# Kernel tuning notes

Hardware: AMD Instinct MI355X
Metric: run time of the kernel (lower is better)

## Reference

```python
import jax, jax.numpy as jnp
import numpy as np

B, S = 128, 32
C = [4, 8, 16, 32]
DN = ('NDHWC', 'DHWIO', 'NDHWC')


def _conv(x, w, stride=1, pad=None):
    k = w.shape[0]
    if pad is None:
        pad = [((k - 1) // 2, k // 2)] * 3  # k=3 -> (1,1); k=4 -> (1,2) as in scn even-kernel convention
    return jax.lax.conv_general_dilated(x, w, (stride,) * 3, pad, dimension_numbers=DN)


def _bn_relu(x, g, b, mask, eps=1e-4):
    # BatchNormLeakyReLU with leakiness=0 (ReLU); stats over ACTIVE voxels only, per channel
    cnt = jnp.maximum(mask.sum(), 1.0)
    mean = (x * mask).sum(axis=(0, 1, 2, 3)) / cnt
    var = (((x - mean) ** 2) * mask).sum(axis=(0, 1, 2, 3)) / cnt
    y = (x - mean) * jax.lax.rsqrt(var + eps) * g + b
    return jnp.maximum(y, 0.0) * mask


def _pool_mask(m):
    # scn.Convolution k=2 s=2: output site active iff any input in its 2^3 receptive field is active
    return jax.lax.reduce_window(m, 0.0, jax.lax.max, (1, 2, 2, 2, 1), (1, 2, 2, 2, 1), 'VALID')


def _up_mask(m):
    # scn.FullConvolution k=2 s=2: each active input activates its full 2^3 output block
    return jnp.repeat(jnp.repeat(jnp.repeat(m, 2, 1), 2, 2), 2, 3)


def _encoder(vox, maskraw, wp, enc, dec, wo):
    mask = (maskraw == 0).astype(vox.dtype)
    x = vox * mask
    x = _conv(x, wp) * mask  # prepare: submanifold conv 1 -> m=4
    for (g, b, ws, wd) in enc:  # 3 non-empty encoding stages (i < num_strides-1)
        x = _bn_relu(x, g, b, mask)
        x = _conv(x, ws) * mask               # submanifold conv k=3
        x = _conv(x, wd, stride=2, pad=[(0, 0)] * 3)  # strided Convolution k=2 s=2
        mask = _pool_mask(mask)
        x = x * mask
    # SparseToDense + view(-1, C*s^3) in NCDHW layout
    hidden = jnp.transpose(x, (0, 4, 1, 2, 3)).reshape(x.shape[0], -1)
    for (g, b, wu, ws3, ws4) in dec:  # i = 2, 1, 0
        x = _bn_relu(x, g, b, mask)
        x = jax.lax.conv_transpose(x, wu, (2, 2, 2), 'VALID', dimension_numbers=DN)  # FullConvolution
        mask = _up_mask(mask)
        x = x * mask
        x = _conv(x, ws3) * mask              # submanifold conv k=3 (end of decoding_conv1)
        mask = mask * (x[..., :1] > 0).astype(x.dtype)  # SparsifyFCS (applied twice; idempotent)
        x = x * mask
        x = _conv(x, ws4) * mask              # submanifold conv k=4 (decoding_conv2)
    out = _conv(x, wo) * mask                 # output: submanifold conv m -> 1
    return hidden, out


def setup_inputs():
    key = jax.random.key(0)
    ks = iter(jax.random.split(key, 64))

    def rnd(shape, s=0.1):
        return jax.random.normal(next(ks), shape, jnp.float32) * s

    inp = {}
    inp['vox'] = jax.random.normal(next(ks), (B, S, S, S, 1), jnp.float32)
    inp['maskraw'] = jax.random.randint(next(ks), (B, S, S, S, 1), 0, 10, jnp.int32)
    inp['wp'] = rnd((3, 3, 3, 1, C[0]))
    for i in range(3):
        ci, co = C[i], C[i + 1]
        inp[f'g_e{i}'] = 1.0 + rnd((ci,))
        inp[f'b_e{i}'] = rnd((ci,))
        inp[f'ws_e{i}'] = rnd((3, 3, 3, ci, ci))
        inp[f'wd_e{i}'] = rnd((2, 2, 2, ci, co))
    for j, i in enumerate([2, 1, 0]):
        ci, co = C[i + 1], C[i]
        inp[f'g_d{j}'] = 1.0 + rnd((ci,))
        inp[f'b_d{j}'] = rnd((ci,))
        inp[f'wu_d{j}'] = rnd((2, 2, 2, ci, co))
        inp[f'ws3_d{j}'] = rnd((3, 3, 3, co, co))
        inp[f'ws4_d{j}'] = rnd((4, 4, 4, co, co))
    inp['wo'] = rnd((3, 3, 3, C[0], 1))
    return inp


def reference(vox, maskraw, wp, g_e0, b_e0, ws_e0, wd_e0, g_e1, b_e1, ws_e1, wd_e1, g_e2, b_e2, ws_e2, wd_e2, g_d0, b_d0, wu_d0, ws3_d0, ws4_d0, g_d1, b_d1, wu_d1, ws3_d1, ws4_d1, g_d2, b_d2, wu_d2, ws3_d2, ws4_d2, wo):
    enc = [(g_e0, b_e0, ws_e0, wd_e0), (g_e1, b_e1, ws_e1, wd_e1), (g_e2, b_e2, ws_e2, wd_e2)]
    dec = [(g_d0, b_d0, wu_d0, ws3_d0, ws4_d0), (g_d1, b_d1, wu_d1, ws3_d1, ws4_d1), (g_d2, b_d2, wu_d2, ws3_d2, ws4_d2)]
    return _encoder(vox, maskraw, wp, enc, dec, wo)
```

## Files before the change

kernel.cpp:

```cpp
#include <hip/hip_runtime.h>

using u8 = unsigned char;

__global__ void mask_init_k(const int* __restrict__ mr, u8* __restrict__ m, int N) {
    int i = blockIdx.x * blockDim.x + threadIdx.x;
    if (i < N) m[i] = (mr[i] == 0) ? 1 : 0;
}

template <int SO>
__global__ void pool_k(const u8* __restrict__ mi, u8* __restrict__ mo) {
    const int N = 128 * SO * SO * SO;
    constexpr int SI = 2 * SO;
    int v = blockIdx.x * blockDim.x + threadIdx.x;
    if (v >= N) return;
    int t = v;
    int x = t % SO; t /= SO;
    int y = t % SO; t /= SO;
    int z = t % SO;
    int n = t / SO;
    u8 m = 0;
    for (int kd = 0; kd < 2; kd++)
        for (int kh = 0; kh < 2; kh++)
            for (int kw = 0; kw < 2; kw++)
                m |= mi[((n * SI + 2 * z + kd) * SI + 2 * y + kh) * SI + 2 * x + kw];
    mo[v] = m;
}


__global__ void prep4t_k(const float* __restrict__ vox, const u8* __restrict__ m,
                         const float* __restrict__ wp, float* __restrict__ out) {
    __shared__ float til[6 * 10 * 35];
    int bid = blockIdx.x;
    int y0 = (bid & 3) << 3, z0 = ((bid >> 2) & 7) << 2, n = bid >> 5;
    for (int t = threadIdx.x; t < 6 * 10 * 35; t += 256) {
        int x_ = t % 35;
        int rr = t / 35;
        int yy = rr % 10, zz = rr / 10;
        int gx = x_ - 1, gy = y0 + yy - 1, gz = z0 + zz - 1;
        float v = 0.f;
        if ((unsigned)gx < 32u && (unsigned)gy < 32u && (unsigned)gz < 32u) {
            int gi = ((n * 32 + gz) * 32 + gy) * 32 + gx;
            if (m[gi]) v = vox[gi];
        }
        til[t] = v;
    }
    __syncthreads();
    int tx = threadIdx.x;
    int xg = tx & 7, ly = (tx >> 3) & 7, lz = tx >> 6;
    int xb = xg << 2;
    int vbase = ((n * 32 + z0 + lz) * 32 + y0 + ly) * 32 + xb;
    u8 om[4];
#pragma unroll
    for (int j = 0; j < 4; j++) om[j] = m[vbase + j];
    float acc[4][4];
#pragma unroll
    for (int j = 0; j < 4; j++)
#pragma unroll
        for (int co = 0; co < 4; co++) acc[j][co] = 0.f;
    for (int kd = 0; kd < 3; kd++) {
        for (int kh = 0; kh < 3; kh++) {
            const float* rowp = &til[((lz + kd) * 10 + ly + kh) * 35 + xb];
            float col[6];
#pragma unroll
            for (int c = 0; c < 6; c++) col[c] = rowp[c];
            const float* wrow = wp + ((kd * 3 + kh) * 3) * 4;
#pragma unroll
            for (int kw = 0; kw < 3; kw++) {
                const float* wt = wrow + kw * 4;
#pragma unroll
                for (int j = 0; j < 4; j++) {
                    float xv = col[j + kw];
#pragma unroll
                    for (int co = 0; co < 4; co++) acc[j][co] += xv * wt[co];
                }
            }
        }
    }
#pragma unroll
    for (int j = 0; j < 4; j++)
#pragma unroll
        for (int co = 0; co < 4; co++)
            out[(size_t)(vbase + j) * 4 + co] = om[j] ? acc[j][co] : 0.f;
}

__global__ void convbn4t_k(const float* __restrict__ in, const float* __restrict__ w,
                           const u8* __restrict__ mask, const double* __restrict__ params,
                           float* __restrict__ out) {
    __shared__ float4 til[6 * 10 * 35];
    float sc[4], sh[4];
#pragma unroll
    for (int c = 0; c < 4; c++) { sc[c] = (float)params[c]; sh[c] = (float)params[4 + c]; }
    int bid = blockIdx.x;
    int y0 = (bid & 3) << 3, z0 = ((bid >> 2) & 7) << 2, n = bid >> 5;
    for (int t = threadIdx.x; t < 6 * 10 * 35; t += 256) {
        int x_ = t % 35;
        int rr = t / 35;
        int yy = rr % 10, zz = rr / 10;
        int gx = x_ - 1, gy = y0 + yy - 1, gz = z0 + zz - 1;
        float4 v = make_float4(0.f, 0.f, 0.f, 0.f);
        if ((unsigned)gx < 32u && (unsigned)gy < 32u && (unsigned)gz < 32u) {
            int gi = ((n * 32 + gz) * 32 + gy) * 32 + gx;
            if (mask[gi]) {
                float4 r = *(const float4*)(in + (size_t)gi * 4);
                v.x = fmaxf(r.x * sc[0] + sh[0], 0.f);
                v.y = fmaxf(r.y * sc[1] + sh[1], 0.f);
                v.z = fmaxf(r.z * sc[2] + sh[2], 0.f);
                v.w = fmaxf(r.w * sc[3] + sh[3], 0.f);
            }
        }
        til[t] = v;
    }
    __syncthreads();
    int tx = threadIdx.x;
    int xg = tx & 7, ly = (tx >> 3) & 7, lz = tx >> 6;
    int xb = xg << 2;
    int vbase = ((n * 32 + z0 + lz) * 32 + y0 + ly) * 32 + xb;
    u8 om[4];
#pragma unroll
    for (int j = 0; j < 4; j++) om[j] = mask[vbase + j];
    float acc[4][4];
#pragma unroll
    for (int j = 0; j < 4; j++)
#pragma unroll
        for (int co = 0; co < 4; co++) acc[j][co] = 0.f;
    for (int kd = 0; kd < 3; kd++) {
        for (int kh = 0; kh < 3; kh++) {
            const float4* rowp = &til[((lz + kd) * 10 + ly + kh) * 35 + xb];
            float col[6][4];
#pragma unroll
            for (int c = 0; c < 6; c++) {
                float4 t4 = rowp[c];
                col[c][0] = t4.x; col[c][1] = t4.y; col[c][2] = t4.z; col[c][3] = t4.w;
            }
            const float* wrow = w + ((kd * 3 + kh) * 3) * 16;
#pragma unroll
            for (int kw = 0; kw < 3; kw++) {
                const float* wt = wrow + kw * 16;
#pragma unroll
                for (int j = 0; j < 4; j++) {
#pragma unroll
                    for (int ci = 0; ci < 4; ci++) {
                        float xv = col[j + kw][ci];
#pragma unroll
                        for (int co = 0; co < 4; co++) acc[j][co] += xv * wt[ci * 4 + co];
                    }
                }
            }
        }
    }
#pragma unroll
    for (int j = 0; j < 4; j++)
#pragma unroll
        for (int co = 0; co < 4; co++)
            out[(size_t)(vbase + j) * 4 + co] = om[j] ? acc[j][co] : 0.f;
}

__global__ void conv3s4t_k(const float* __restrict__ in, const float* __restrict__ w,
                           const u8* __restrict__ pmask, u8* __restrict__ nmask,
                           float* __restrict__ out, double delta) {
    __shared__ float4 til[6 * 10 * 35];
    int bid = blockIdx.x;
    int y0 = (bid & 3) << 3, z0 = ((bid >> 2) & 7) << 2, n = bid >> 5;
    for (int t = threadIdx.x; t < 6 * 10 * 35; t += 256) {
        int x_ = t % 35;
        int rr = t / 35;
        int yy = rr % 10, zz = rr / 10;
        int gx = x_ - 1, gy = y0 + yy - 1, gz = z0 + zz - 1;
        float4 v = make_float4(0.f, 0.f, 0.f, 0.f);
        if ((unsigned)gx < 32u && (unsigned)gy < 32u && (unsigned)gz < 32u)
            v = *(const float4*)(in + (size_t)(((n * 32 + gz) * 32 + gy) * 32 + gx) * 4);
        til[t] = v;
    }
    __syncthreads();
    int tx = threadIdx.x;
    int xg = tx & 7, ly = (tx >> 3) & 7, lz = tx >> 6;
    int xb = xg << 2;
    int gy = y0 + ly, gz = z0 + lz;
    int vbase = ((n * 32 + gz) * 32 + gy) * 32 + xb;
    int pbase = ((n * 16 + (gz >> 1)) * 16 + (gy >> 1)) * 16 + (xb >> 1);
    u8 pm[4];
    pm[0] = pm[1] = pmask[pbase];
    pm[2] = pm[3] = pmask[pbase + 1];
    double acc0[4], asum[4];
    float accf[4][4];
#pragma unroll
    for (int j = 0; j < 4; j++) {
        acc0[j] = 0.0; asum[j] = 0.0;
#pragma unroll
        for (int co = 0; co < 4; co++) accf[j][co] = 0.f;
    }
    for (int kd = 0; kd < 3; kd++) {
        for (int kh = 0; kh < 3; kh++) {
            const float4* rowp = &til[((lz + kd) * 10 + ly + kh) * 35 + xb];
            float col[6][4];
#pragma unroll
            for (int c = 0; c < 6; c++) {
                float4 t4 = rowp[c];
                col[c][0] = t4.x; col[c][1] = t4.y; col[c][2] = t4.z; col[c][3] = t4.w;
            }
            const float* wrow = w + ((kd * 3 + kh) * 3) * 16;
#pragma unroll
            for (int kw = 0; kw < 3; kw++) {
                const float* wt = wrow + kw * 16;
#pragma unroll
                for (int j = 0; j < 4; j++) {
#pragma unroll
                    for (int ci = 0; ci < 4; ci++) {
                        float xv = col[j + kw][ci];
                        double term = (double)xv * (double)wt[ci * 4 + 0];
                        acc0[j] += term;
                        asum[j] += fabs(term);
#pragma unroll
                        for (int co = 1; co < 4; co++) accf[j][co] += xv * wt[ci * 4 + co];
                    }
                }
            }
        }
    }
#pragma unroll
    for (int j = 0; j < 4; j++) {
        u8 nm = (pm[j] && (acc0[j] > -delta * asum[j])) ? 1 : 0;
        nmask[vbase + j] = nm;
        out[(size_t)(vbase + j) * 4 + 0] = nm ? (float)acc0[j] : 0.f;
#pragma unroll
        for (int co = 1; co < 4; co++) out[(size_t)(vbase + j) * 4 + co] = nm ? accf[j][co] : 0.f;
    }
}

__global__ void conv4x4t_k(const float* __restrict__ in, const float* __restrict__ w,
                           const u8* __restrict__ outmask, float* __restrict__ out) {
    __shared__ float4 til[7 * 11 * 35];
    int bid = blockIdx.x;
    int y0 = (bid & 3) << 3, z0 = ((bid >> 2) & 7) << 2, n = bid >> 5;
    for (int t = threadIdx.x; t < 7 * 11 * 35; t += 256) {
        int x_ = t % 35;
        int rr = t / 35;
        int yy = rr % 11, zz = rr / 11;
        int gx = x_ - 1, gy = y0 + yy - 1, gz = z0 + zz - 1;
        float4 v = make_float4(0.f, 0.f, 0.f, 0.f);
        if ((unsigned)gx < 32u && (unsigned)gy < 32u && (unsigned)gz < 32u)
            v = *(const float4*)(in + (size_t)(((n * 32 + gz) * 32 + gy) * 32 + gx) * 4);
        til[t] = v;
    }
    __syncthreads();
    int tx = threadIdx.x;
    int xg = tx & 7, ly = (tx >> 3) & 7, lz = tx >> 6;
    int xb = xg << 2;
    int vbase = ((n * 32 + z0 + lz) * 32 + y0 + ly) * 32 + xb;
    u8 om[4];
#pragma unroll
    for (int j = 0; j < 4; j++) om[j] = outmask[vbase + j];
    float acc[4][4];
#pragma unroll
    for (int j = 0; j < 4; j++)
#pragma unroll
        for (int co = 0; co < 4; co++) acc[j][co] = 0.f;
    for (int kd = 0; kd < 4; kd++) {
        for (int kh = 0; kh < 4; kh++) {
            const float4* rowp = &til[((lz + kd) * 11 + ly + kh) * 35 + xb];
            float col[7][4];
#pragma unroll
            for (int c = 0; c < 7; c++) {
                float4 t4 = rowp[c];
                col[c][0] = t4.x; col[c][1] = t4.y; col[c][2] = t4.z; col[c][3] = t4.w;
            }
            const float* wrow = w + ((kd * 4 + kh) * 4) * 16;
#pragma unroll
            for (int kw = 0; kw < 4; kw++) {
                const float* wt = wrow + kw * 16;
#pragma unroll
                for (int j = 0; j < 4; j++) {
#pragma unroll
                    for (int ci = 0; ci < 4; ci++) {
                        float xv = col[j + kw][ci];
#pragma unroll
                        for (int co = 0; co < 4; co++) acc[j][co] += xv * wt[ci * 4 + co];
                    }
                }
            }
        }
    }
#pragma unroll
    for (int j = 0; j < 4; j++)
#pragma unroll
        for (int co = 0; co < 4; co++)
            out[(size_t)(vbase + j) * 4 + co] = om[j] ? acc[j][co] : 0.f;
}

__global__ void outconv4t_k(const float* __restrict__ in, const float* __restrict__ w,
                            const u8* __restrict__ mask, float* __restrict__ out) {
    __shared__ float4 til[6 * 10 * 35];
    int bid = blockIdx.x;
    int y0 = (bid & 3) << 3, z0 = ((bid >> 2) & 7) << 2, n = bid >> 5;
    for (int t = threadIdx.x; t < 6 * 10 * 35; t += 256) {
        int x_ = t % 35;
        int rr = t / 35;
        int yy = rr % 10, zz = rr / 10;
        int gx = x_ - 1, gy = y0 + yy - 1, gz = z0 + zz - 1;
        float4 v = make_float4(0.f, 0.f, 0.f, 0.f);
        if ((unsigned)gx < 32u && (unsigned)gy < 32u && (unsigned)gz < 32u)
            v = *(const float4*)(in + (size_t)(((n * 32 + gz) * 32 + gy) * 32 + gx) * 4);
        til[t] = v;
    }
    __syncthreads();
    int tx = threadIdx.x;
    int xg = tx & 7, ly = (tx >> 3) & 7, lz = tx >> 6;
    int xb = xg << 2;
    int vbase = ((n * 32 + z0 + lz) * 32 + y0 + ly) * 32 + xb;
    u8 om[4];
#pragma unroll
    for (int j = 0; j < 4; j++) om[j] = mask[vbase + j];
    float acc[4] = {0.f, 0.f, 0.f, 0.f};
    for (int kd = 0; kd < 3; kd++) {
        for (int kh = 0; kh < 3; kh++) {
            const float4* rowp = &til[((lz + kd) * 10 + ly + kh) * 35 + xb];
            float col[6][4];
#pragma unroll
            for (int c = 0; c < 6; c++) {
                float4 t4 = rowp[c];
                col[c][0] = t4.x; col[c][1] = t4.y; col[c][2] = t4.z; col[c][3] = t4.w;
            }
            const float* wrow = w + ((kd * 3 + kh) * 3) * 4;
#pragma unroll
            for (int kw = 0; kw < 3; kw++) {
                const float* wt = wrow + kw * 4;
#pragma unroll
                for (int j = 0; j < 4; j++) {
#pragma unroll
                    for (int ci = 0; ci < 4; ci++) acc[j] += col[j + kw][ci] * wt[ci];
                }
            }
        }
    }
#pragma unroll
    for (int j = 0; j < 4; j++) out[vbase + j] = om[j] ? acc[j] : 0.f;
}


__global__ void convbn8_k(const float* __restrict__ in, const float* __restrict__ w,
                          const u8* __restrict__ mask, const double* __restrict__ params,
                          float* __restrict__ out) {
    __shared__ float til[3 * 10 * 11 * 16];
    float sc[16], sh[16];
#pragma unroll
    for (int c = 0; c < 16; c++) { sc[c] = (float)params[c]; sh[c] = (float)params[16 + c]; }
    int z = blockIdx.x & 7, n = blockIdx.x >> 3;
    for (int t = threadIdx.x; t < 300; t += 64) {
        int xx = t % 10;
        int rr = t / 10;
        int yy = rr % 10, zz = rr / 10;
        int gx = xx - 1, gy = yy - 1, gz = z + zz - 1;
        float v[16];
#pragma unroll
        for (int c = 0; c < 16; c++) v[c] = 0.f;
        if ((unsigned)gx < 8u && (unsigned)gy < 8u && (unsigned)gz < 8u) {
            int gi = ((n * 8 + gz) * 8 + gy) * 8 + gx;
            if (mask[gi]) {
                const float* ip = in + (size_t)gi * 16;
#pragma unroll
                for (int c = 0; c < 16; c++) v[c] = fmaxf(ip[c] * sc[c] + sh[c], 0.f);
            }
        }
        float* dst = &til[((zz * 10 + yy) * 11 + xx) * 16];
#pragma unroll
        for (int k = 0; k < 4; k++)
            ((float4*)dst)[k] = make_float4(v[4 * k], v[4 * k + 1], v[4 * k + 2], v[4 * k + 3]);
    }
    __syncthreads();
    int x = threadIdx.x & 7, y = threadIdx.x >> 3;
    int v = ((n * 8 + z) * 8 + y) * 8 + x;
    u8 om = mask[v];
    float acc[16];
#pragma unroll
    for (int co = 0; co < 16; co++) acc[co] = 0.f;
    for (int kd = 0; kd < 3; kd++) {
        for (int kh = 0; kh < 3; kh++) {
            const float* rp = &til[((kd * 10 + (y + kh)) * 11 + x) * 16];
#pragma unroll
            for (int kw = 0; kw < 3; kw++) {
                const float* xp = rp + kw * 16;
                const float* wt = w + ((kd * 3 + kh) * 3 + kw) * 256;
#pragma unroll
                for (int ci = 0; ci < 16; ci++) {
                    float xv = xp[ci];
#pragma unroll
                    for (int co = 0; co < 16; co++) acc[co] += xv * wt[ci * 16 + co];
                }
            }
        }
    }
#pragma unroll
    for (int co = 0; co < 16; co++) out[(size_t)v * 16 + co] = om ? acc[co] : 0.f;
}

__global__ void conv3s8_k(const float* __restrict__ in, const float* __restrict__ w,
                          const u8* __restrict__ pmask, u8* __restrict__ nmask,
                          float* __restrict__ out, double delta) {
    __shared__ float til[3 * 10 * 11 * 16];
    int z = blockIdx.x & 7, n = blockIdx.x >> 3;
    for (int t = threadIdx.x; t < 300; t += 64) {
        int xx = t % 10;
        int rr = t / 10;
        int yy = rr % 10, zz = rr / 10;
        int gx = xx - 1, gy = yy - 1, gz = z + zz - 1;
        float4 v0 = make_float4(0.f, 0.f, 0.f, 0.f), v1 = v0, v2 = v0, v3 = v0;
        if ((unsigned)gx < 8u && (unsigned)gy < 8u && (unsigned)gz < 8u) {
            const float4* ip = (const float4*)(in + (size_t)(((n * 8 + gz) * 8 + gy) * 8 + gx) * 16);
            v0 = ip[0]; v1 = ip[1]; v2 = ip[2]; v3 = ip[3];
        }
        float4* dst = (float4*)&til[((zz * 10 + yy) * 11 + xx) * 16];
        dst[0] = v0; dst[1] = v1; dst[2] = v2; dst[3] = v3;
    }
    __syncthreads();
    int x = threadIdx.x & 7, y = threadIdx.x >> 3;
    int v = ((n * 8 + z) * 8 + y) * 8 + x;
    int pidx = ((n * 4 + (z >> 1)) * 4 + (y >> 1)) * 4 + (x >> 1);
    u8 pm = pmask[pidx];
    double acc0 = 0.0, asum = 0.0;
    float accf[16];
#pragma unroll
    for (int co = 0; co < 16; co++) accf[co] = 0.f;
    for (int kd = 0; kd < 3; kd++) {
        for (int kh = 0; kh < 3; kh++) {
            const float* rp = &til[((kd * 10 + (y + kh)) * 11 + x) * 16];
#pragma unroll
            for (int kw = 0; kw < 3; kw++) {
                const float* xp = rp + kw * 16;
                const float* wt = w + ((kd * 3 + kh) * 3 + kw) * 256;
#pragma unroll
                for (int ci = 0; ci < 16; ci++) {
                    float xv = xp[ci];
                    double term = (double)xv * (double)wt[ci * 16 + 0];
                    acc0 += term;
                    asum += fabs(term);
#pragma unroll
                    for (int co = 1; co < 16; co++) accf[co] += xv * wt[ci * 16 + co];
                }
            }
        }
    }
    u8 nm = (pm && (acc0 > -delta * asum)) ? 1 : 0;
    nmask[v] = nm;
    out[(size_t)v * 16 + 0] = nm ? (float)acc0 : 0.f;
#pragma unroll
    for (int co = 1; co < 16; co++) out[(size_t)v * 16 + co] = nm ? accf[co] : 0.f;
}

__global__ void conv48_k(const float* __restrict__ in, const float* __restrict__ w,
                         const u8* __restrict__ outmask, float* __restrict__ out) {
    __shared__ float til[4 * 11 * 13 * 16];
    int z = blockIdx.x & 7, n = blockIdx.x >> 3;
    for (int t = threadIdx.x; t < 484; t += 64) {
        int xx = t % 11;
        int rr = t / 11;
        int yy = rr % 11, zz = rr / 11;
        int gx = xx - 1, gy = yy - 1, gz = z + zz - 1;
        float4 v0 = make_float4(0.f, 0.f, 0.f, 0.f), v1 = v0, v2 = v0, v3 = v0;
        if ((unsigned)gx < 8u && (unsigned)gy < 8u && (unsigned)gz < 8u) {
            const float4* ip = (const float4*)(in + (size_t)(((n * 8 + gz) * 8 + gy) * 8 + gx) * 16);
            v0 = ip[0]; v1 = ip[1]; v2 = ip[2]; v3 = ip[3];
        }
        float4* dst = (float4*)&til[((zz * 11 + yy) * 13 + xx) * 16];
        dst[0] = v0; dst[1] = v1; dst[2] = v2; dst[3] = v3;
    }
    __syncthreads();
    int x = threadIdx.x & 7, y = threadIdx.x >> 3;
    int v = ((n * 8 + z) * 8 + y) * 8 + x;
    u8 om = outmask[v];
    float acc[16];
#pragma unroll
    for (int co = 0; co < 16; co++) acc[co] = 0.f;
    for (int kd = 0; kd < 4; kd++) {
        for (int kh = 0; kh < 4; kh++) {
            const float* rp = &til[((kd * 11 + (y + kh)) * 13 + x) * 16];
#pragma unroll
            for (int kw = 0; kw < 4; kw++) {
                const float* xp = rp + kw * 16;
                const float* wt = w + ((kd * 4 + kh) * 4 + kw) * 256;
#pragma unroll
                for (int ci = 0; ci < 16; ci++) {
                    float xv = xp[ci];
#pragma unroll
                    for (int co = 0; co < 16; co++) acc[co] += xv * wt[ci * 16 + co];
                }
            }
        }
    }
#pragma unroll
    for (int co = 0; co < 16; co++) out[(size_t)v * 16 + co] = om ? acc[co] : 0.f;
}


template <int K, int CIN, int COUT, int S>
__global__ void conv_k(const float* __restrict__ in, const float* __restrict__ w,
                       const u8* __restrict__ outmask, float* __restrict__ out) {
    const int N = 128 * S * S * S;
    int v = blockIdx.x * blockDim.x + threadIdx.x;
    if (v >= N) return;
    if (!outmask[v]) {
#pragma unroll
        for (int co = 0; co < COUT; co++) out[(size_t)v * COUT + co] = 0.f;
        return;
    }
    int t = v;
    int x = t % S; t /= S;
    int y = t % S; t /= S;
    int z = t % S;
    int n = t / S;
    float acc[COUT];
#pragma unroll
    for (int co = 0; co < COUT; co++) acc[co] = 0.f;
    constexpr int PLO = (K - 1) / 2;
    for (int kd = 0; kd < K; kd++) {
        int zz = z + kd - PLO; if ((unsigned)zz >= (unsigned)S) continue;
        for (int kh = 0; kh < K; kh++) {
            int yy = y + kh - PLO; if ((unsigned)yy >= (unsigned)S) continue;
            for (int kw = 0; kw < K; kw++) {
                int xx = x + kw - PLO; if ((unsigned)xx >= (unsigned)S) continue;
                int sv = ((n * S + zz) * S + yy) * S + xx;
                const float* ip = in + (size_t)sv * CIN;
                const float* wpk = w + ((kd * K + kh) * K + kw) * CIN * COUT;
#pragma unroll
                for (int ci = 0; ci < CIN; ci++) {
                    float xv = ip[ci];
#pragma unroll
                    for (int co = 0; co < COUT; co++) acc[co] += xv * wpk[ci * COUT + co];
                }
            }
        }
    }
#pragma unroll
    for (int co = 0; co < COUT; co++) out[(size_t)v * COUT + co] = acc[co];
}

template <int CIN, int COUT, int S>
__global__ void convbn_k(const float* __restrict__ in, const float* __restrict__ w,
                         const u8* __restrict__ mask, const double* __restrict__ params,
                         float* __restrict__ out) {
    const int N = 128 * S * S * S;
    int v = blockIdx.x * blockDim.x + threadIdx.x;
    if (v >= N) return;
    if (!mask[v]) {
#pragma unroll
        for (int co = 0; co < COUT; co++) out[(size_t)v * COUT + co] = 0.f;
        return;
    }
    int t = v;
    int x = t % S; t /= S;
    int y = t % S; t /= S;
    int z = t % S;
    int n = t / S;
    float sc[CIN], sh[CIN];
#pragma unroll
    for (int c = 0; c < CIN; c++) { sc[c] = (float)params[c]; sh[c] = (float)params[CIN + c]; }
    float acc[COUT];
#pragma unroll
    for (int co = 0; co < COUT; co++) acc[co] = 0.f;
    for (int kd = 0; kd < 3; kd++) {
        int zz = z + kd - 1; if ((unsigned)zz >= (unsigned)S) continue;
        for (int kh = 0; kh < 3; kh++) {
            int yy = y + kh - 1; if ((unsigned)yy >= (unsigned)S) continue;
            for (int kw = 0; kw < 3; kw++) {
                int xx = x + kw - 1; if ((unsigned)xx >= (unsigned)S) continue;
                int sv = ((n * S + zz) * S + yy) * S + xx;
                if (!mask[sv]) continue;
                const float* ip = in + (size_t)sv * CIN;
                const float* wpk = w + ((kd * 3 + kh) * 3 + kw) * CIN * COUT;
#pragma unroll
                for (int ci = 0; ci < CIN; ci++) {
                    float yv = fmaxf(ip[ci] * sc[ci] + sh[ci], 0.f);
#pragma unroll
                    for (int co = 0; co < COUT; co++) acc[co] += yv * wpk[ci * COUT + co];
                }
            }
        }
    }
#pragma unroll
    for (int co = 0; co < COUT; co++) out[(size_t)v * COUT + co] = acc[co];
}

template <int CIN, int COUT, int S>
__global__ void conv3s_k(const float* __restrict__ in, const float* __restrict__ w,
                         const u8* __restrict__ pmask, u8* __restrict__ nmask,
                         float* __restrict__ out, double delta) {
    const int N = 128 * S * S * S;
    constexpr int SP = S / 2;
    int v = blockIdx.x * blockDim.x + threadIdx.x;
    if (v >= N) return;
    int t = v;
    int x = t % S; t /= S;
    int y = t % S; t /= S;
    int z = t % S;
    int n = t / S;
    int pidx = ((n * SP + (z >> 1)) * SP + (y >> 1)) * SP + (x >> 1);
    if (!pmask[pidx]) {
        nmask[v] = 0;
#pragma unroll
        for (int co = 0; co < COUT; co++) out[(size_t)v * COUT + co] = 0.f;
        return;
    }
    double acc0 = 0.0, asum = 0.0;
    float acc[COUT];
#pragma unroll
    for (int co = 0; co < COUT; co++) acc[co] = 0.f;
    for (int kd = 0; kd < 3; kd++) {
        int zz = z + kd - 1; if ((unsigned)zz >= (unsigned)S) continue;
        for (int kh = 0; kh < 3; kh++) {
            int yy = y + kh - 1; if ((unsigned)yy >= (unsigned)S) continue;
            for (int kw = 0; kw < 3; kw++) {
                int xx = x + kw - 1; if ((unsigned)xx >= (unsigned)S) continue;
                int sv = ((n * S + zz) * S + yy) * S + xx;
                const float* ip = in + (size_t)sv * CIN;
                const float* wpk = w + ((kd * 3 + kh) * 3 + kw) * CIN * COUT;
#pragma unroll
                for (int ci = 0; ci < CIN; ci++) {
                    float xv = ip[ci];
                    double term = (double)xv * (double)wpk[ci * COUT + 0];
                    acc0 += term;
                    asum += fabs(term);
#pragma unroll
                    for (int co = 1; co < COUT; co++) acc[co] += xv * wpk[ci * COUT + co];
                }
            }
        }
    }
    u8 nm = (acc0 > -delta * asum) ? 1 : 0;
    nmask[v] = nm;
    out[(size_t)v * COUT + 0] = nm ? (float)acc0 : 0.f;
#pragma unroll
    for (int co = 1; co < COUT; co++) out[(size_t)v * COUT + co] = nm ? acc[co] : 0.f;
}

template <int CIN, int COUT, int SO>
__global__ void down_k(const float* __restrict__ in, const float* __restrict__ w,
                       const u8* __restrict__ outmask, float* __restrict__ out) {
    const int N = 128 * SO * SO * SO;
    constexpr int SI = 2 * SO;
    int v = blockIdx.x * blockDim.x + threadIdx.x;
    if (v >= N) return;
    if (!outmask[v]) {
#pragma unroll
        for (int co = 0; co < COUT; co++) out[(size_t)v * COUT + co] = 0.f;
        return;
    }
    int t = v;
    int x = t % SO; t /= SO;
    int y = t % SO; t /= SO;
    int z = t % SO;
    int n = t / SO;
    float acc[COUT];
#pragma unroll
    for (int co = 0; co < COUT; co++) acc[co] = 0.f;
    for (int kd = 0; kd < 2; kd++)
        for (int kh = 0; kh < 2; kh++)
            for (int kw = 0; kw < 2; kw++) {
                int sv = ((n * SI + 2 * z + kd) * SI + 2 * y + kh) * SI + 2 * x + kw;
                const float* ip = in + (size_t)sv * CIN;
                const float* wpk = w + ((kd * 2 + kh) * 2 + kw) * CIN * COUT;
#pragma unroll
                for (int ci = 0; ci < CIN; ci++) {
                    float xv = ip[ci];
#pragma unroll
                    for (int co = 0; co < COUT; co++) acc[co] += xv * wpk[ci * COUT + co];
                }
            }
#pragma unroll
    for (int co = 0; co < COUT; co++) out[(size_t)v * COUT + co] = acc[co];
}

template <int CIN, int COUT, int SI>
__global__ void upbn_k(const float* __restrict__ in, const float* __restrict__ w,
                       const u8* __restrict__ inmask, const double* __restrict__ params,
                       float* __restrict__ out) {
    constexpr int SO = 2 * SI;
    const int N = 128 * SO * SO * SO;
    int v = blockIdx.x * blockDim.x + threadIdx.x;
    if (v >= N) return;
    int t = v;
    int x = t % SO; t /= SO;
    int y = t % SO; t /= SO;
    int z = t % SO;
    int n = t / SO;
    int sv = ((n * SI + (z >> 1)) * SI + (y >> 1)) * SI + (x >> 1);
    if (!inmask[sv]) {
#pragma unroll
        for (int co = 0; co < COUT; co++) out[(size_t)v * COUT + co] = 0.f;
        return;
    }
    int tap = ((1 - (z & 1)) * 2 + (1 - (y & 1))) * 2 + (1 - (x & 1));
    const float* wpk = w + tap * CIN * COUT;
    const float* ip = in + (size_t)sv * CIN;
    float acc[COUT];
#pragma unroll
    for (int co = 0; co < COUT; co++) acc[co] = 0.f;
#pragma unroll
    for (int ci = 0; ci < CIN; ci++) {
        float yv = fmaxf(ip[ci] * (float)params[ci] + (float)params[CIN + ci], 0.f);
#pragma unroll
        for (int co = 0; co < COUT; co++) acc[co] += yv * wpk[ci * COUT + co];
    }
#pragma unroll
    for (int co = 0; co < COUT; co++) out[(size_t)v * COUT + co] = acc[co];
}

template <int C>
__global__ void bn_reduce_k(const float* __restrict__ x, const u8* __restrict__ m, int N,
                            double* __restrict__ partial) {
    double cnt = 0.0, sx[C], s2[C];
#pragma unroll
    for (int c = 0; c < C; c++) { sx[c] = 0.0; s2[c] = 0.0; }
    int stride = gridDim.x * blockDim.x;
    for (int v = blockIdx.x * blockDim.x + threadIdx.x; v < N; v += stride) {
        if (!m[v]) continue;
        cnt += 1.0;
#pragma unroll
        for (int c = 0; c < C; c++) {
            double xv = (double)x[(size_t)v * C + c];
            sx[c] += xv;
            s2[c] += xv * xv;
        }
    }
#pragma unroll
    for (int off = 32; off > 0; off >>= 1) {
        cnt += __shfl_down(cnt, off, 64);
#pragma unroll
        for (int c = 0; c < C; c++) {
            sx[c] += __shfl_down(sx[c], off, 64);
            s2[c] += __shfl_down(s2[c], off, 64);
        }
    }
    __shared__ double sbuf[4][2 * C + 1];
    int wave = threadIdx.x >> 6;
    if ((threadIdx.x & 63) == 0) {
        sbuf[wave][0] = cnt;
#pragma unroll
        for (int c = 0; c < C; c++) {
            sbuf[wave][1 + c] = sx[c];
            sbuf[wave][1 + C + c] = s2[c];
        }
    }
    __syncthreads();
    if (threadIdx.x == 0) {
        double* p = partial + (size_t)blockIdx.x * (2 * C + 1);
        double tcnt = 0.0;
        for (int wv = 0; wv < 4; wv++) tcnt += sbuf[wv][0];
        p[0] = tcnt;
#pragma unroll
        for (int c = 0; c < C; c++) {
            double a = 0.0, b = 0.0;
            for (int wv = 0; wv < 4; wv++) { a += sbuf[wv][1 + c]; b += sbuf[wv][1 + C + c]; }
            p[1 + c] = a;
            p[1 + C + c] = b;
        }
    }
}

template <int C>
__global__ void bn_final_k(const double* __restrict__ partial, int nblocks,
                           const float* __restrict__ g, const float* __restrict__ b,
                           double* __restrict__ params) {
    int c = threadIdx.x;
    if (c >= C) return;
    double cnt = 0.0, sx = 0.0, s2 = 0.0;
    for (int bk = 0; bk < nblocks; bk++) {
        const double* p = partial + (size_t)bk * (2 * C + 1);
        cnt += p[0];
        sx += p[1 + c];
        s2 += p[1 + C + c];
    }
    if (cnt < 1.0) cnt = 1.0;
    double mean = sx / cnt;
    double var = s2 / cnt - mean * mean;
    double sc = (double)g[c] / sqrt(var + 1e-4);
    params[c] = sc;
    params[C + c] = (double)b[c] - mean * sc;
}

__global__ void hidden_k(const float* __restrict__ x, float* __restrict__ out) {
    int i = blockIdx.x * blockDim.x + threadIdx.x;
    if (i >= 128 * 2048) return;
    int b = i >> 11;
    int r = i & 2047;
    int c = r >> 6;
    int s = r & 63;
    int d = s >> 4;
    int h = (s >> 2) & 3;
    int w = s & 3;
    out[i] = x[((((b * 4 + d) * 4 + h) * 4 + w) << 5) + c];
}

extern "C" void kernel_launch(void* const* d_in, const int* in_sizes, int n_in,
                              void* d_out, int out_size, void* d_ws, size_t ws_size,
                              hipStream_t stream) {
    const float* vox = (const float*)d_in[0];
    const int* mraw = (const int*)d_in[1];
    const float* wp = (const float*)d_in[2];
    const float* g_e0 = (const float*)d_in[3];
    const float* b_e0 = (const float*)d_in[4];
    const float* ws_e0 = (const float*)d_in[5];
    const float* wd_e0 = (const float*)d_in[6];
    const float* g_e1 = (const float*)d_in[7];
    const float* b_e1 = (const float*)d_in[8];
    const float* ws_e1 = (const float*)d_in[9];
    const float* wd_e1 = (const float*)d_in[10];
    const float* g_e2 = (const float*)d_in[11];
    const float* b_e2 = (const float*)d_in[12];
    const float* ws_e2 = (const float*)d_in[13];
    const float* wd_e2 = (const float*)d_in[14];
    const float* g_d0 = (const float*)d_in[15];
    const float* b_d0 = (const float*)d_in[16];
    const float* wu_d0 = (const float*)d_in[17];
    const float* ws3_d0 = (const float*)d_in[18];
    const float* ws4_d0 = (const float*)d_in[19];
    const float* g_d1 = (const float*)d_in[20];
    const float* b_d1 = (const float*)d_in[21];
    const float* wu_d1 = (const float*)d_in[22];
    const float* ws3_d1 = (const float*)d_in[23];
    const float* ws4_d1 = (const float*)d_in[24];
    const float* g_d2 = (const float*)d_in[25];
    const float* b_d2 = (const float*)d_in[26];
    const float* wu_d2 = (const float*)d_in[27];
    const float* ws3_d2 = (const float*)d_in[28];
    const float* ws4_d2 = (const float*)d_in[29];
    const float* wo = (const float*)d_in[30];
    float* out = (float*)d_out;

    float* wsf = (float*)d_ws;
    size_t offf = 0;
    auto allocf = [&](size_t n) { float* p = wsf + offf; offf += n; return p; };
    float* R1 = allocf(16777216);
    float* R2 = allocf(16777216);
    float* S1 = allocf(1048576);
    float* S2 = allocf(1048576);
    float* T = allocf(262144);
    double* wsd = (double*)(wsf + offf);
    double* partial = wsd;
    double* params = wsd + 16640;
    u8* wsm = (u8*)(wsd + 16640 + 128);
    size_t offm = 0;
    auto allocm = [&](size_t n) { u8* p = wsm + offm; offm += n; return p; };
    u8* m32 = allocm(4194304);
    u8* m16 = allocm(524288);
    u8* m8 = allocm(65536);
    u8* m4 = allocm(8192);
    u8* mD8 = allocm(65536);
    u8* mD16 = allocm(524288);
    u8* mD32 = allocm(4194304);

    const int N32 = 128 * 32768;
    const int N16 = 128 * 4096;
    const int N8 = 128 * 512;
    const int N4 = 128 * 64;
    auto gs = [](int n) { return dim3((n + 255) / 256); };
    auto rbn = [](int n) { int bl = (n + 255) / 256; return bl > 256 ? 256 : bl; };
    dim3 blk(256);
    dim3 tgrid(4096);
    dim3 grid8(1024);
    dim3 blk64(64);

    mask_init_k<<<gs(N32), blk, 0, stream>>>(mraw, m32, N32);
    pool_k<16><<<gs(N16), blk, 0, stream>>>(m32, m16);
    pool_k<8><<<gs(N8), blk, 0, stream>>>(m16, m8);
    pool_k<4><<<gs(N4), blk, 0, stream>>>(m8, m4);

    prep4t_k<<<tgrid, blk, 0, stream>>>(vox, m32, wp, R1);
    int nb0 = rbn(N32);
    bn_reduce_k<4><<<dim3(nb0), blk, 0, stream>>>(R1, m32, N32, partial);
    bn_final_k<4><<<1, 64, 0, stream>>>(partial, nb0, g_e0, b_e0, params);
    convbn4t_k<<<tgrid, blk, 0, stream>>>(R1, ws_e0, m32, params, R2);
    down_k<4, 8, 16><<<gs(N16), blk, 0, stream>>>(R2, wd_e0, m16, R1);

    int nb1 = rbn(N16);
    bn_reduce_k<8><<<dim3(nb1), blk, 0, stream>>>(R1, m16, N16, partial);
    bn_final_k<8><<<1, 64, 0, stream>>>(partial, nb1, g_e1, b_e1, params);
    convbn_k<8, 8, 16><<<gs(N16), blk, 0, stream>>>(R1, ws_e1, m16, params, R2);
    down_k<8, 16, 8><<<gs(N8), blk, 0, stream>>>(R2, wd_e1, m8, S1);

    int nb2 = rbn(N8);
    bn_reduce_k<16><<<dim3(nb2), blk, 0, stream>>>(S1, m8, N8, partial);
    bn_final_k<16><<<1, 64, 0, stream>>>(partial, nb2, g_e2, b_e2, params);
    convbn8_k<<<grid8, blk64, 0, stream>>>(S1, ws_e2, m8, params, S2);
    down_k<16, 32, 4><<<gs(N4), blk, 0, stream>>>(S2, wd_e2, m4, T);

    hidden_k<<<gs(128 * 2048), blk, 0, stream>>>(T, out);

    int nb3 = rbn(N4);
    bn_reduce_k<32><<<dim3(nb3), blk, 0, stream>>>(T, m4, N4, partial);
    bn_final_k<32><<<1, 64, 0, stream>>>(partial, nb3, g_d0, b_d0, params);
    upbn_k<32, 16, 4><<<gs(N8), blk, 0, stream>>>(T, wu_d0, m4, params, S1);
    conv3s8_k<<<grid8, blk64, 0, stream>>>(S1, ws3_d0, m4, mD8, S2, 4e-7);
    conv48_k<<<grid8, blk64, 0, stream>>>(S2, ws4_d0, mD8, S1);

    int nb4 = rbn(N8);
    bn_reduce_k<16><<<dim3(nb4), blk, 0, stream>>>(S1, mD8, N8, partial);
    bn_final_k<16><<<1, 64, 0, stream>>>(partial, nb4, g_d1, b_d1, params);
    upbn_k<16, 8, 8><<<gs(N16), blk, 0, stream>>>(S1, wu_d1, mD8, params, R1);
    conv3s_k<8, 8, 16><<<gs(N16), blk, 0, stream>>>(R1, ws3_d1, mD8, mD16, R2, 4e-7);
    conv_k<4, 8, 8, 16><<<gs(N16), blk, 0, stream>>>(R2, ws4_d1, mD16, R1);

    int nb5 = rbn(N16);
    bn_reduce_k<8><<<dim3(nb5), blk, 0, stream>>>(R1, mD16, N16, partial);
    bn_final_k<8><<<1, 64, 0, stream>>>(partial, nb5, g_d2, b_d2, params);
    upbn_k<8, 4, 16><<<gs(N32), blk, 0, stream>>>(R1, wu_d2, mD16, params, R2);
    conv3s4t_k<<<tgrid, blk, 0, stream>>>(R2, ws3_d2, mD16, mD32, R1, 0.0);
    conv4x4t_k<<<tgrid, blk, 0, stream>>>(R1, ws4_d2, mD32, R2);
    outconv4t_k<<<tgrid, blk, 0, stream>>>(R2, wo, mD32, out + 262144);
}
```

Measured before the change: 1.576 ms.

## Split output channels across four thread groups in 8^3 conv kernels

The three 8^3-resolution convolution kernels now run 256 threads per block instead of 64. Each group of 64 threads computes a quarter of the 16 output channels, so per-thread accumulator registers drop and occupancy rises. The shared tile is reorganised into four float4 channel planes to reduce bank conflicts. In the sparsify kernel, only the first channel group computes the double-precision channel-0 sum, and the resulting mask is shared with the other groups through shared memory and an extra barrier. The cost is that each group re-reads the same input tile, and groups in that kernel diverge.

```diff
diff --git a/kernel.cpp b/kernel.cpp
--- a/kernel.cpp
+++ b/kernel.cpp
@@ -340,12 +340,12 @@
 __global__ void convbn8_k(const float* __restrict__ in, const float* __restrict__ w,
                           const u8* __restrict__ mask, const double* __restrict__ params,
                           float* __restrict__ out) {
-    __shared__ float til[3 * 10 * 11 * 16];
+    __shared__ float4 til[4][330];
     float sc[16], sh[16];
 #pragma unroll
     for (int c = 0; c < 16; c++) { sc[c] = (float)params[c]; sh[c] = (float)params[16 + c]; }
     int z = blockIdx.x & 7, n = blockIdx.x >> 3;
-    for (int t = threadIdx.x; t < 300; t += 64) {
+    for (int t = threadIdx.x; t < 300; t += 256) {
         int xx = t % 10;
         int rr = t / 10;
         int yy = rr % 10, zz = rr / 10;
@@ -361,44 +361,49 @@
                 for (int c = 0; c < 16; c++) v[c] = fmaxf(ip[c] * sc[c] + sh[c], 0.f);
             }
         }
-        float* dst = &til[((zz * 10 + yy) * 11 + xx) * 16];
-#pragma unroll
-        for (int k = 0; k < 4; k++)
-            ((float4*)dst)[k] = make_float4(v[4 * k], v[4 * k + 1], v[4 * k + 2], v[4 * k + 3]);
+        int s = (zz * 10 + yy) * 11 + xx;
+#pragma unroll
+        for (int q = 0; q < 4; q++)
+            til[q][s] = make_float4(v[4 * q], v[4 * q + 1], v[4 * q + 2], v[4 * q + 3]);
     }
     __syncthreads();
-    int x = threadIdx.x & 7, y = threadIdx.x >> 3;
+    int x = threadIdx.x & 7, y = (threadIdx.x >> 3) & 7, cq = threadIdx.x >> 6;
     int v = ((n * 8 + z) * 8 + y) * 8 + x;
     u8 om = mask[v];
-    float acc[16];
-#pragma unroll
-    for (int co = 0; co < 16; co++) acc[co] = 0.f;
+    float acc[4] = {0.f, 0.f, 0.f, 0.f};
     for (int kd = 0; kd < 3; kd++) {
         for (int kh = 0; kh < 3; kh++) {
-            const float* rp = &til[((kd * 10 + (y + kh)) * 11 + x) * 16];
+            int rbase = (kd * 10 + y + kh) * 11 + x;
+            const float* wrow = w + ((kd * 3 + kh) * 3) * 256;
 #pragma unroll
             for (int kw = 0; kw < 3; kw++) {
-                const float* xp = rp + kw * 16;
-                const float* wt = w + ((kd * 3 + kh) * 3 + kw) * 256;
+                int s = rbase + kw;
+                float4 q0 = til[0][s], q1 = til[1][s], q2 = til[2][s], q3 = til[3][s];
+                float xs[16] = {q0.x, q0.y, q0.z, q0.w, q1.x, q1.y, q1.z, q1.w,
+                                q2.x, q2.y, q2.z, q2.w, q3.x, q3.y, q3.z, q3.w};
+                const float* wt = wrow + kw * 256 + cq * 4;
 #pragma unroll
                 for (int ci = 0; ci < 16; ci++) {
-                    float xv = xp[ci];
-#pragma unroll
-                    for (int co = 0; co < 16; co++) acc[co] += xv * wt[ci * 16 + co];
-                }
-            }
-        }
-    }
-#pragma unroll
-    for (int co = 0; co < 16; co++) out[(size_t)v * 16 + co] = om ? acc[co] : 0.f;
+                    float xv = xs[ci];
+                    float4 w4 = *(const float4*)(wt + ci * 16);
+                    acc[0] += xv * w4.x; acc[1] += xv * w4.y;
+                    acc[2] += xv * w4.z; acc[3] += xv * w4.w;
+                }
+            }
+        }
+    }
+    float* op = out + (size_t)v * 16 + cq * 4;
+#pragma unroll
+    for (int j = 0; j < 4; j++) op[j] = om ? acc[j] : 0.f;
 }
 
 __global__ void conv3s8_k(const float* __restrict__ in, const float* __restrict__ w,
                           const u8* __restrict__ pmask, u8* __restrict__ nmask,
                           float* __restrict__ out, double delta) {
-    __shared__ float til[3 * 10 * 11 * 16];
+    __shared__ float4 til[4][330];
+    __shared__ u8 nmsh[64];
     int z = blockIdx.x & 7, n = blockIdx.x >> 3;
-    for (int t = threadIdx.x; t < 300; t += 64) {
+    for (int t = threadIdx.x; t < 300; t += 256) {
         int xx = t % 10;
         int rr = t / 10;
         int yy = rr % 10, zz = rr / 10;
@@ -408,49 +413,72 @@
             const float4* ip = (const float4*)(in + (size_t)(((n * 8 + gz) * 8 + gy) * 8 + gx) * 16);
             v0 = ip[0]; v1 = ip[1]; v2 = ip[2]; v3 = ip[3];
         }
-        float4* dst = (float4*)&til[((zz * 10 + yy) * 11 + xx) * 16];
-        dst[0] = v0; dst[1] = v1; dst[2] = v2; dst[3] = v3;
+        int s = (zz * 10 + yy) * 11 + xx;
+        til[0][s] = v0; til[1][s] = v1; til[2][s] = v2; til[3][s] = v3;
     }
     __syncthreads();
-    int x = threadIdx.x & 7, y = threadIdx.x >> 3;
+    int x = threadIdx.x & 7, y = (threadIdx.x >> 3) & 7, cq = threadIdx.x >> 6;
     int v = ((n * 8 + z) * 8 + y) * 8 + x;
-    int pidx = ((n * 4 + (z >> 1)) * 4 + (y >> 1)) * 4 + (x >> 1);
-    u8 pm = pmask[pidx];
     double acc0 = 0.0, asum = 0.0;
-    float accf[16];
-#pragma unroll
-    for (int co = 0; co < 16; co++) accf[co] = 0.f;
+    float acc[4] = {0.f, 0.f, 0.f, 0.f};
     for (int kd = 0; kd < 3; kd++) {
         for (int kh = 0; kh < 3; kh++) {
-            const float* rp = &til[((kd * 10 + (y + kh)) * 11 + x) * 16];
+            int rbase = (kd * 10 + y + kh) * 11 + x;
+            const float* wrow = w + ((kd * 3 + kh) * 3) * 256;
 #pragma unroll
             for (int kw = 0; kw < 3; kw++) {
-                const float* xp = rp + kw * 16;
-                const float* wt = w + ((kd * 3 + kh) * 3 + kw) * 256;
-#pragma unroll
-                for (int ci = 0; ci < 16; ci++) {
-                    float xv = xp[ci];
-                    double term = (double)xv * (double)wt[ci * 16 + 0];
-                    acc0 += term;
-                    asum += fabs(term);
-#pragma unroll
-                    for (int co = 1; co < 16; co++) accf[co] += xv * wt[ci * 16 + co];
-                }
-            }
-        }
-    }
-    u8 nm = (pm && (acc0 > -delta * asum)) ? 1 : 0;
-    nmask[v] = nm;
-    out[(size_t)v * 16 + 0] = nm ? (float)acc0 : 0.f;
-#pragma unroll
-    for (int co = 1; co < 16; co++) out[(size_t)v * 16 + co] = nm ? accf[co] : 0.f;
+                int s = rbase + kw;
+                float4 q0 = til[0][s], q1 = til[1][s], q2 = til[2][s], q3 = til[3][s];
+                float xs[16] = {q0.x, q0.y, q0.z, q0.w, q1.x, q1.y, q1.z, q1.w,
+                                q2.x, q2.y, q2.z, q2.w, q3.x, q3.y, q3.z, q3.w};
+                const float* wt0 = wrow + kw * 256;
+                if (cq == 0) {
+#pragma unroll
+                    for (int ci = 0; ci < 16; ci++) {
+                        float xv = xs[ci];
+                        double term = (double)xv * (double)wt0[ci * 16];
+                        acc0 += term;
+                        asum += fabs(term);
+#pragma unroll
+                        for (int j = 1; j < 4; j++) acc[j] += xv * wt0[ci * 16 + j];
+                    }
+                } else {
+                    const float* wt = wt0 + cq * 4;
+#pragma unroll
+                    for (int ci = 0; ci < 16; ci++) {
+                        float xv = xs[ci];
+                        float4 w4 = *(const float4*)(wt + ci * 16);
+                        acc[0] += xv * w4.x; acc[1] += xv * w4.y;
+                        acc[2] += xv * w4.z; acc[3] += xv * w4.w;
+                    }
+                }
+            }
+        }
+    }
+    if (cq == 0) {
+        u8 pm = pmask[((n * 4 + (z >> 1)) * 4 + (y >> 1)) * 4 + (x >> 1)];
+        u8 nm = (pm && (acc0 > -delta * asum)) ? 1 : 0;
+        nmsh[y * 8 + x] = nm;
+        nmask[v] = nm;
+    }
+    __syncthreads();
+    u8 nm = nmsh[y * 8 + x];
+    float* op = out + (size_t)v * 16 + cq * 4;
+    if (cq == 0) {
+        op[0] = nm ? (float)acc0 : 0.f;
+#pragma unroll
+        for (int j = 1; j < 4; j++) op[j] = nm ? acc[j] : 0.f;
+    } else {
+#pragma unroll
+        for (int j = 0; j < 4; j++) op[j] = nm ? acc[j] : 0.f;
+    }
 }
 
 __global__ void conv48_k(const float* __restrict__ in, const float* __restrict__ w,
                          const u8* __restrict__ outmask, float* __restrict__ out) {
-    __shared__ float til[4 * 11 * 13 * 16];
+    __shared__ float4 til[4][572];
     int z = blockIdx.x & 7, n = blockIdx.x >> 3;
-    for (int t = threadIdx.x; t < 484; t += 64) {
+    for (int t = threadIdx.x; t < 484; t += 256) {
         int xx = t % 11;
         int rr = t / 11;
         int yy = rr % 11, zz = rr / 11;
@@ -460,34 +488,38 @@
             const float4* ip = (const float4*)(in + (size_t)(((n * 8 + gz) * 8 + gy) * 8 + gx) * 16);
             v0 = ip[0]; v1 = ip[1]; v2 = ip[2]; v3 = ip[3];
         }
-        float4* dst = (float4*)&til[((zz * 11 + yy) * 13 + xx) * 16];
-        dst[0] = v0; dst[1] = v1; dst[2] = v2; dst[3] = v3;
+        int s = (zz * 11 + yy) * 13 + xx;
+        til[0][s] = v0; til[1][s] = v1; til[2][s] = v2; til[3][s] = v3;
     }
     __syncthreads();
-    int x = threadIdx.x & 7, y = threadIdx.x >> 3;
+    int x = threadIdx.x & 7, y = (threadIdx.x >> 3) & 7, cq = threadIdx.x >> 6;
     int v = ((n * 8 + z) * 8 + y) * 8 + x;
     u8 om = outmask[v];
-    float acc[16];
-#pragma unroll
-    for (int co = 0; co < 16; co++) acc[co] = 0.f;
+    float acc[4] = {0.f, 0.f, 0.f, 0.f};
     for (int kd = 0; kd < 4; kd++) {
         for (int kh = 0; kh < 4; kh++) {
-            const float* rp = &til[((kd * 11 + (y + kh)) * 13 + x) * 16];
+            int rbase = (kd * 11 + y + kh) * 13 + x;
+            const float* wrow = w + ((kd * 4 + kh) * 4) * 256;
 #pragma unroll
             for (int kw = 0; kw < 4; kw++) {
-                const float* xp = rp + kw * 16;
-                const float* wt = w + ((kd * 4 + kh) * 4 + kw) * 256;
+                int s = rbase + kw;
+                float4 q0 = til[0][s], q1 = til[1][s], q2 = til[2][s], q3 = til[3][s];
+                float xs[16] = {q0.x, q0.y, q0.z, q0.w, q1.x, q1.y, q1.z, q1.w,
+                                q2.x, q2.y, q2.z, q2.w, q3.x, q3.y, q3.z, q3.w};
+                const float* wt = wrow + kw * 256 + cq * 4;
 #pragma unroll
                 for (int ci = 0; ci < 16; ci++) {
-                    float xv = xp[ci];
-#pragma unroll
-                    for (int co = 0; co < 16; co++) acc[co] += xv * wt[ci * 16 + co];
-                }
-            }
-        }
-    }
-#pragma unroll
-    for (int co = 0; co < 16; co++) out[(size_t)v * 16 + co] = om ? acc[co] : 0.f;
+                    float xv = xs[ci];
+                    float4 w4 = *(const float4*)(wt + ci * 16);
+                    acc[0] += xv * w4.x; acc[1] += xv * w4.y;
+                    acc[2] += xv * w4.z; acc[3] += xv * w4.w;
+                }
+            }
+        }
+    }
+    float* op = out + (size_t)v * 16 + cq * 4;
+#pragma unroll
+    for (int j = 0; j < 4; j++) op[j] = om ? acc[j] : 0.f;
 }
 
 
@@ -856,7 +888,6 @@
     dim3 blk(256);
     dim3 tgrid(4096);
     dim3 grid8(1024);
-    dim3 blk64(64);
 
     mask_init_k<<<gs(N32), blk, 0, stream>>>(mraw, m32, N32);
     pool_k<16><<<gs(N16), blk, 0, stream>>>(m32, m16);
@@ -879,7 +910,7 @@
     int nb2 = rbn(N8);
     bn_reduce_k<16><<<dim3(nb2), blk, 0, stream>>>(S1, m8, N8, partial);
     bn_final_k<16><<<1, 64, 0, stream>>>(partial, nb2, g_e2, b_e2, params);
-    convbn8_k<<<grid8, blk64, 0, stream>>>(S1, ws_e2, m8, params, S2);
+    convbn8_k<<<grid8, blk, 0, stream>>>(S1, ws_e2, m8, params, S2);
     down_k<16, 32, 4><<<gs(N4), blk, 0, stream>>>(S2, wd_e2, m4, T);
 
     hidden_k<<<gs(128 * 2048), blk, 0, stream>>>(T, out);
@@ -888,8 +919,8 @@
     bn_reduce_k<32><<<dim3(nb3), blk, 0, stream>>>(T, m4, N4, partial);
     bn_final_k<32><<<1, 64, 0, stream>>>(partial, nb3, g_d0, b_d0, params);
     upbn_k<32, 16, 4><<<gs(N8), blk, 0, stream>>>(T, wu_d0, m4, params, S1);
-    conv3s8_k<<<grid8, blk64, 0, stream>>>(S1, ws3_d0, m4, mD8, S2, 4e-7);
-    conv48_k<<<grid8, blk64, 0, stream>>>(S2, ws4_d0, mD8, S1);
+    conv3s8_k<<<grid8, blk, 0, stream>>>(S1, ws3_d0, m4, mD8, S2, 4e-7);
+    conv48_k<<<grid8, blk, 0, stream>>>(S2, ws4_d0, mD8, S1);
 
     int nb4 = rbn(N8);
     bn_reduce_k<16><<<dim3(nb4), blk, 0, stream>>>(S1, mD8, N8, partial);
```

New measurement: 1.444 ms. 8.4% less time.
